# Optimization experiments

Measured on AMD Instinct MI355X. Metric: run time of the kernel, lower is better.

## Reference

```python
import jax, jax.numpy as jnp
import numpy as np

N, E = 20000, 320000
CS, CV = 64, 32          # scalar / vector multiplicities of node (= node_pre) irreps
AS_, AV, H = 16, 8, 4    # attn irreps scalar/vector muls, num_heads
NB = 16                  # num_basis
SQRT3 = 1.7320508075688772
SQRT2 = 1.4142135623730951
EPS = 1e-5

# dtp weight layout: [ss(CS), sv(CS), vs(CV), vv0(CV), vv1(CV)] -> numel = 2*CS+3*CV = 224

def _cg_tp(s, v, y0, y1, w_ss, w_sv, w_vs, w_vv0, w_vv1):
    """Depthwise CG tensor product for l<=1.
    s:(E,CS) v:(E,CV,3) y0:(E,) y1:(E,3); weights (E,C) or (C,).
    out scalars (E, CS+CV): 0e x 0e -> 0e, 1o x 1o -> 0e (dot/sqrt3)
    out vectors (E, CS+2*CV, 3): 0e x 1o -> 1o, 1o x 0e -> 1o, 1o x 1o -> 1o (cross/sqrt2)
    """
    out_s = jnp.concatenate([
        w_ss * s * y0[:, None],
        w_vv0 * (jnp.einsum('eci,ei->ec', v, y1) / SQRT3)], axis=-1)
    out_v = jnp.concatenate([
        (w_sv * s)[:, :, None] * y1[:, None, :],
        (w_vs * jnp.ones_like(v[..., 0]))[..., None] * v * y0[:, None, None],
        (w_vv1 * jnp.ones_like(v[..., 0]))[..., None] * (jnp.cross(v, y1[:, None, :]) / SQRT2)], axis=1)
    return out_s, out_v


def _equiv_layernorm(s, v, gamma_s, beta_s, gamma_v):
    mu = jnp.mean(s, axis=-1, keepdims=True)
    var = jnp.var(s, axis=-1, keepdims=True)
    s_n = (s - mu) * jax.lax.rsqrt(var + EPS) * gamma_s + beta_s
    rms = jnp.sqrt(jnp.mean(jnp.sum(v * v, axis=-1), axis=-1, keepdims=True) + EPS)
    v_n = v / rms[..., None] * gamma_v[None, :, None]
    return s_n, v_n


def setup_inputs() -> dict:
    key = jax.random.key(0)
    ks = jax.random.split(key, 26)
    def rn(k, shape, fan):
        return jax.random.normal(k, shape, jnp.float32) / np.sqrt(fan)
    D1S, D1V = CS + CV, CS + 2 * CV          # 96, 128 (dtp output muls)
    WN = 2 * CS + 3 * CV                     # 224 dtp weight numel
    inp = {
        'node': jax.random.normal(ks[0], (N, CS + 3 * CV), jnp.float32),
        'edge_index': jax.random.randint(ks[1], (2, E), 0, N, jnp.int64 if jax.config.jax_enable_x64 else jnp.int32),
        'rbf': jax.random.uniform(ks[2], (E, NB), jnp.float32),
        'rsh': jax.random.normal(ks[3], (E, 4), jnp.float32),
        'gamma_s': jnp.ones((CS,), jnp.float32),
        'beta_s': jnp.zeros((CS,), jnp.float32),
        'gamma_v': jnp.ones((CV,), jnp.float32),
        'Ws_src': rn(ks[4], (CS, CS), CS), 'Wv_src': rn(ks[5], (CV, CV), CV),
        'Ws_dst': rn(ks[6], (CS, CS), CS), 'Wv_dst': rn(ks[7], (CV, CV), CV),
        'W_rbf': rn(ks[8], (NB, WN), NB),
        'W_alpha': rn(ks[9], (D1S, H * AS_), D1S),
        'alpha_dot': rn(ks[10], (1, H, AS_), AS_),
        'Ws_val': rn(ks[11], (D1S, CS), D1S), 'Wv_val': rn(ks[12], (D1V, CV), D1V),
        'Wg': rn(ks[13], (CS, CV), CS),
        'w2_ss': rn(ks[14], (CS,), 1), 'w2_sv': rn(ks[15], (CS,), 1),
        'w2_vs': rn(ks[16], (CV,), 1), 'w2_vv0': rn(ks[17], (CV,), 1), 'w2_vv1': rn(ks[18], (CV,), 1),
        'Ws_vlin': rn(ks[19], (D1S, H * AS_), D1S), 'Wv_vlin': rn(ks[20], (D1V, H * AV), D1V),
        'Wps': rn(ks[21], (H * AS_, CS), H * AS_), 'Wpv': rn(ks[22], (H * AV, CV), H * AV),
    }
    return inp


def reference(node, rbf, rsh, gamma_s, beta_s, gamma_v, Ws_src, Wv_src, Ws_dst, Wv_dst,
              W_rbf, W_alpha, alpha_dot, Ws_val, Wv_val, Wg,
              w2_ss, w2_sv, w2_vs, w2_vv0, w2_vv1, Ws_vlin, Wv_vlin, Wps, Wpv, edge_index):
    n = node.shape[0]
    e = rsh.shape[0]
    s = node[:, :CS]
    v = node[:, CS:].reshape(n, CV, 3)
    # equivariant layer norm
    s_n, v_n = _equiv_layernorm(s, v, gamma_s, beta_s, gamma_v)
    # merge_src / merge_dst (irrep-wise o3.Linear)
    src, dst = edge_index[0], edge_index[1]
    msg_s = (s_n @ Ws_src)[src] + (s_n @ Ws_dst)[dst]                       # (E,CS)
    msg_v = jnp.einsum('ncx,cd->ndx', v_n, Wv_src)[src] + \
            jnp.einsum('ncx,cd->ndx', v_n, Wv_dst)[dst]                     # (E,CV,3)
    y0, y1 = rsh[:, 0], rsh[:, 1:4]
    # dtp1: per-edge weighted CG coupling, weights from rbf
    w1 = rbf @ W_rbf                                                        # (E,224)
    m1_s, m1_v = _cg_tp(msg_s, msg_v, y0, y1,
                        w1[:, :CS], w1[:, CS:2*CS], w1[:, 2*CS:2*CS+CV],
                        w1[:, 2*CS+CV:2*CS+2*CV], w1[:, 2*CS+2*CV:])        # (E,96) (E,128,3)
    # attention logits
    a = (m1_s @ W_alpha).reshape(e, H, AS_)
    a = jnp.where(a > 0, a, 0.2 * a)                                        # LeakyReLU(0.2)
    a = jnp.sum(a * alpha_dot, axis=-1, keepdims=True)                      # (E,H,1)
    # softmax over incoming edges of each destination node
    amax = jax.ops.segment_max(a, dst, num_segments=n)
    amax = jnp.where(jnp.isfinite(amax), amax, 0.0)
    ex = jnp.exp(a - amax[dst])
    den = jax.ops.segment_sum(ex, dst, num_segments=n)
    alpha = ex / (den[dst] + 1e-16)                                         # (E,H,1)
    # value path
    val_s = m1_s @ Ws_val                                                   # (E,CS)
    val_v = jnp.einsum('ecx,cd->edx', m1_v, Wv_val)                         # (E,CV,3)
    # gate: sigmoid on scalars, vectors gated by sigmoid of learned scalar gates
    val_v = val_v * jax.nn.sigmoid(val_s @ Wg)[..., None]
    val_s = jax.nn.sigmoid(val_s)
    # dtp2: shared internal weights
    m2_s, m2_v = _cg_tp(val_s, val_v, y0, y1, w2_ss, w2_sv, w2_vs, w2_vv0, w2_vv1)
    # value_lin -> (attn_irreps * num_heads), head-major layout
    hs = (m2_s @ Ws_vlin).reshape(e, H, AS_)
    hv = jnp.einsum('ecx,cd->edx', m2_v, Wv_vlin).reshape(e, H, AV, 3)
    h = jnp.concatenate([hs, hv.reshape(e, H, AV * 3)], axis=-1)            # (E,H,40)
    # attend + scatter-add to destination nodes
    agg = jax.ops.segment_sum(alpha * h, dst, num_segments=n)               # (N,H,40)
    agg_s = agg[:, :, :AS_].reshape(n, H * AS_)                             # (N,64)
    agg_v = agg[:, :, AS_:].reshape(n, H * AV, 3)                           # (N,32,3)
    out = node + jnp.concatenate([
        agg_s @ Wps,
        jnp.einsum('ncx,cd->ndx', agg_v, Wpv).reshape(n, CV * 3)], axis=-1)
    return out
```

## Files before the change

kernel.cpp:

```cpp
#include <hip/hip_runtime.h>
#include <hip/hip_bf16.h>
#include <cstddef>

typedef __hip_bfloat16 bf16;
typedef __bf16 bfv8 __attribute__((ext_vector_type(8)));
typedef float f4 __attribute__((ext_vector_type(4)));

#define EPSN 1e-5f
#define SQRT3_INV 0.57735026918962576f
#define SQRT2_INV 0.70710678118654752f

__device__ __forceinline__ float b2f(bf16 x) { return __bfloat162float(x); }

template<int BF> __device__ __forceinline__ float ldf(const void* p, size_t i) {
    if (BF) return __bfloat162float(((const bf16*)p)[i]);
    return ((const float*)p)[i];
}
__device__ __forceinline__ float ldr(const void* p, size_t i, int bfm) {
    return bfm ? __bfloat162float(((const bf16*)p)[i]) : ((const float*)p)[i];
}
template<int BF> __device__ __forceinline__ void stf(void* p, size_t i, float v) {
    if (BF) ((bf16*)p)[i] = __float2bfloat16(v);
    else    ((float*)p)[i] = v;
}

__device__ __forceinline__ float wave_sum64(float x) {
    #pragma unroll
    for (int m = 1; m < 64; m <<= 1) x += __shfl_xor(x, m, 64);
    return x;
}

__device__ __forceinline__ f4 mf(bfv8 a, bfv8 b, f4 c) {
    return __builtin_amdgcn_mfma_f32_16x16x32_bf16(a, b, c, 0, 0, 0);
}

__global__ __launch_bounds__(256) void k_sniff(const void* node, const void* eidx, int* flags)
{
    int t = threadIdx.x;
    __shared__ int cnt;
    __shared__ unsigned orr;
    if (t == 0) { cnt = 0; orr = 0u; }
    __syncthreads();
    unsigned w  = ((const unsigned*)node)[t];
    unsigned lo = w & 0xFFFFu;
    int e_lo = (int)((lo >> 7) & 0xFF);
    if (e_lo >= 96 && e_lo <= 140) atomicAdd(&cnt, 1);
    unsigned odd = ((const unsigned*)eidx)[2 * t + 1];
    atomicOr(&orr, odd);
    __syncthreads();
    if (t == 0) {
        flags[0] = (cnt >= 128) ? 1 : 0;
        flags[1] = (orr == 0u) ? 1 : 0;
    }
}

__global__ __launch_bounds__(256) void k_zero(float* p, int n)
{
    int i = blockIdx.x * 256 + threadIdx.x;
    if (i < n) p[i] = 0.f;
}

__global__ __launch_bounds__(256) void k_hist(const void* eidx, int* cnt,
                                              const int* flags, int E)
{
    int e = blockIdx.x * 256 + threadIdx.x;
    if (e >= E) return;
    int d = flags[1] ? (int)((const long long*)eidx)[(long long)E + e]
                     : ((const int*)eidx)[(size_t)E + e];
    atomicAdd(&cnt[d], 1);
}

__global__ __launch_bounds__(256) void k_scan(int* cnt, int N)
{
    __shared__ int part[256];
    int t = threadIdx.x;
    int chunk = (N + 255) / 256;
    int lo = t * chunk, hi = lo + chunk; if (hi > N) hi = N; if (lo > N) lo = N;
    int sum = 0;
    for (int i = lo; i < hi; ++i) sum += cnt[i];
    part[t] = sum;
    __syncthreads();
    if (t == 0) {
        int acc = 0;
        for (int i = 0; i < 256; ++i) { int v = part[i]; part[i] = acc; acc += v; }
    }
    __syncthreads();
    int acc = part[t];
    for (int i = lo; i < hi; ++i) { int v = cnt[i]; cnt[i] = acc; acc += v; }
}

__global__ __launch_bounds__(256) void k_perm(const void* eidx, int* cnt, int* perm,
                                              const int* flags, int E)
{
    int e = blockIdx.x * 256 + threadIdx.x;
    if (e >= E) return;
    int d = flags[1] ? (int)((const long long*)eidx)[(long long)E + e]
                     : ((const int*)eidx)[(size_t)E + e];
    int pos = atomicAdd(&cnt[d], 1);
    perm[pos] = e;
}

template<int BF>
__device__ __forceinline__ void prep_impl(
    const void* Walpha, const void* Wsval, const void* Wsvlin,
    const void* Wvval, const void* Wvvlin, const void* Wg,
    const void* Wrbf, const void* adot,
    const void* w2ss, const void* w2sv, const void* w2vs,
    const void* w2vv0, const void* w2vv1,
    bf16* WalphaT, bf16* WsvalT, bf16* WsvlinT,
    bf16* WvvalT, bf16* WvvlinT, bf16* WgT,
    bf16* WrbfT, bf16* adotB, bf16* w2B)
{
    int t = threadIdx.x + blockIdx.x * 256;
    int T = gridDim.x * 256;
    for (int i = t; i < 96 * 64; i += T) {
        int c = i >> 6, n = i & 63;
        WalphaT[n * 96 + c] = __float2bfloat16(ldf<BF>(Walpha, i));
        WsvalT [n * 96 + c] = __float2bfloat16(ldf<BF>(Wsval,  i));
        WsvlinT[n * 96 + c] = __float2bfloat16(ldf<BF>(Wsvlin, i));
    }
    for (int i = t; i < 128 * 32; i += T) {
        int c = i >> 5, n = i & 31;
        WvvalT [n * 128 + c] = __float2bfloat16(ldf<BF>(Wvval,  i));
        WvvlinT[n * 128 + c] = __float2bfloat16(ldf<BF>(Wvvlin, i));
    }
    for (int i = t; i < 64 * 32; i += T) {
        int c = i >> 5, n = i & 31;
        WgT[n * 64 + c] = __float2bfloat16(ldf<BF>(Wg, i));
    }
    for (int i = t; i < 16 * 224; i += T) {
        int b = i / 224, c = i - b * 224;
        WrbfT[c * 16 + b] = __float2bfloat16(ldf<BF>(Wrbf, i));
    }
    if (t < 64) adotB[t] = __float2bfloat16(ldf<BF>(adot, t));
    if (t < 64) w2B[t]      = __float2bfloat16(ldf<BF>(w2ss, t));
    if (t < 64) w2B[64 + t] = __float2bfloat16(ldf<BF>(w2sv, t));
    if (t < 32) {
        w2B[128 + t] = __float2bfloat16(ldf<BF>(w2vs, t));
        w2B[160 + t] = __float2bfloat16(ldf<BF>(w2vv0, t));
        w2B[192 + t] = __float2bfloat16(ldf<BF>(w2vv1, t));
    }
}

__global__ __launch_bounds__(256) void k_prep(
    const void* Walpha, const void* Wsval, const void* Wsvlin,
    const void* Wvval, const void* Wvvlin, const void* Wg,
    const void* Wrbf, const void* adot,
    const void* w2ss, const void* w2sv, const void* w2vs,
    const void* w2vv0, const void* w2vv1,
    bf16* WalphaT, bf16* WsvalT, bf16* WsvlinT,
    bf16* WvvalT, bf16* WvvlinT, bf16* WgT,
    bf16* WrbfT, bf16* adotB, bf16* w2B, const int* flags)
{
    if (flags[0])
        prep_impl<1>(Walpha, Wsval, Wsvlin, Wvval, Wvvlin, Wg, Wrbf, adot,
                     w2ss, w2sv, w2vs, w2vv0, w2vv1,
                     WalphaT, WsvalT, WsvlinT, WvvalT, WvvlinT, WgT, WrbfT, adotB, w2B);
    else
        prep_impl<0>(Walpha, Wsval, Wsvlin, Wvval, Wvvlin, Wg, Wrbf, adot,
                     w2ss, w2sv, w2vs, w2vv0, w2vv1,
                     WalphaT, WsvalT, WsvlinT, WvvalT, WvvlinT, WgT, WrbfT, adotB, w2B);
}

template<int BF>
__device__ __forceinline__ void node_impl(
    const void* node, const void* gs, const void* bs, const void* gv,
    const void* Wss, const void* Wvs, const void* Wsd, const void* Wvd,
    bf16* ssrc, bf16* sdst, bf16* vsrc, bf16* vdst,
    float* shs, float* shv, int n, int lane)
{
    size_t nb = (size_t)n * 160;

    float s  = ldf<BF>(node, nb + lane);
    float mu = wave_sum64(s) * (1.f / 64.f);
    float d  = s - mu;
    float var = wave_sum64(d * d) * (1.f / 64.f);
    float sn  = d * rsqrtf(var + EPSN) * ldf<BF>(gs, lane) + ldf<BF>(bs, lane);
    shs[lane] = sn;

    float v0 = 0.f, v1 = 0.f, v2 = 0.f, q = 0.f;
    if (lane < 32) {
        v0 = ldf<BF>(node, nb + 64 + lane * 3 + 0);
        v1 = ldf<BF>(node, nb + 64 + lane * 3 + 1);
        v2 = ldf<BF>(node, nb + 64 + lane * 3 + 2);
        q = v0 * v0 + v1 * v1 + v2 * v2;
    }
    float msq = wave_sum64(q) * (1.f / 32.f);
    float inv = rsqrtf(msq + EPSN);
    if (lane < 32) {
        float g = ldf<BF>(gv, lane);
        shv[0 * 32 + lane] = v0 * inv * g;
        shv[1 * 32 + lane] = v1 * inv * g;
        shv[2 * 32 + lane] = v2 * inv * g;
    }

    float a1 = 0.f, a2 = 0.f;
    for (int c = 0; c < 64; ++c) {
        float sc = shs[c];
        a1 += sc * ldf<BF>(Wss, c * 64 + lane);
        a2 += sc * ldf<BF>(Wsd, c * 64 + lane);
    }
    ssrc[(size_t)n * 64 + lane] = __float2bfloat16(a1);
    sdst[(size_t)n * 64 + lane] = __float2bfloat16(a2);

    {
        int x = lane >> 5, dd = lane & 31;
        float p1 = 0.f, p2 = 0.f;
        for (int c = 0; c < 32; ++c) {
            float vc = shv[x * 32 + c];
            p1 += vc * ldf<BF>(Wvs, c * 32 + dd);
            p2 += vc * ldf<BF>(Wvd, c * 32 + dd);
        }
        vsrc[(size_t)n * 96 + x * 32 + dd] = __float2bfloat16(p1);
        vdst[(size_t)n * 96 + x * 32 + dd] = __float2bfloat16(p2);
    }
    if (lane < 32) {
        int dd = lane;
        float p1 = 0.f, p2 = 0.f;
        for (int c = 0; c < 32; ++c) {
            float vc = shv[2 * 32 + c];
            p1 += vc * ldf<BF>(Wvs, c * 32 + dd);
            p2 += vc * ldf<BF>(Wvd, c * 32 + dd);
        }
        vsrc[(size_t)n * 96 + 64 + dd] = __float2bfloat16(p1);
        vdst[(size_t)n * 96 + 64 + dd] = __float2bfloat16(p2);
    }
}

__global__ __launch_bounds__(256) void k_node(
    const void* node, const void* gs, const void* bs, const void* gv,
    const void* Wss, const void* Wvs, const void* Wsd, const void* Wvd,
    bf16* ssrc, bf16* sdst, bf16* vsrc, bf16* vdst,
    const int* flags, int N)
{
    __shared__ float shs[4][64];
    __shared__ float shv[4][96];
    int wv = threadIdx.x >> 6, lane = threadIdx.x & 63;
    int n = blockIdx.x * 4 + wv; if (n >= N) return;
    if (flags[0])
        node_impl<1>(node, gs, bs, gv, Wss, Wvs, Wsd, Wvd, ssrc, sdst, vsrc, vdst,
                     shs[wv], shv[wv], n, lane);
    else
        node_impl<0>(node, gs, bs, gv, Wss, Wvs, Wsd, Wvd, ssrc, sdst, vsrc, vdst,
                     shs[wv], shv[wv], n, lane);
}

static constexpr int A1S = 0,    SS = 104;
static constexpr int A1V = 1664, PV = 2176, SV = 136;
static constexpr int VAL = 8192, SA = 72;
static constexpr int HSZ = 9344;

__global__ __launch_bounds__(256, 2) void k_edge(
    const void* __restrict__ eidx, const void* __restrict__ rbf, const void* __restrict__ rsh,
    const bf16* __restrict__ WalphaT, const bf16* __restrict__ WsvalT, const bf16* __restrict__ WsvlinT,
    const bf16* __restrict__ WvvalT, const bf16* __restrict__ WvvlinT, const bf16* __restrict__ WgT,
    const bf16* __restrict__ WrbfT, const bf16* __restrict__ adotB, const bf16* __restrict__ w2B,
    const bf16* __restrict__ ssrc, const bf16* __restrict__ sdst,
    const bf16* __restrict__ vsrc, const bf16* __restrict__ vdst,
    const int* __restrict__ perm,
    float* __restrict__ den, float* __restrict__ agg,
    const int* __restrict__ flags, int E)
{
    const int bfm = flags[0];
    const int i64 = flags[1];

    __shared__ __align__(16) __bf16 sH[4][HSZ];
    __shared__ __align__(16) float sRbf[4][16][20];
    __shared__ __align__(16) float sY[4][16][4];
    __shared__ int sSD[4][48];

    int wv = threadIdx.x >> 6, l = threadIdx.x & 63;
    int q = l >> 4, m = l & 15;
    long long eb = ((long long)blockIdx.x * 4 + wv) * 16;
    if (eb >= E) return;
    __bf16* H = &sH[wv][0];

    if (l < 16) {
        long long p = eb + l; if (p > (long long)E - 1) p = E - 1;
        sSD[wv][32 + l] = perm[p];
    }
    if (l < 32) {
        int pe = sSD[wv][32 + (l & 15)];
        long long off = (l < 16) ? (long long)pe : ((long long)E + pe);
        sSD[wv][l] = i64 ? (int)((const long long*)eidx)[off] : ((const int*)eidx)[off];
    }
    {
        int pe = sSD[wv][32 + (l >> 2)];
        sY[wv][l >> 2][l & 3] = ldr(rsh, (size_t)pe * 4 + (l & 3), bfm);
    }
    #pragma unroll
    for (int j = 0; j < 4; ++j) {
        int pe = sSD[wv][32 + j * 4 + q];
        sRbf[wv][m][j * 4 + q] = ldr(rbf, (size_t)pe * 16 + m, bfm);
    }

    const __bf16* wrt = (const __bf16*)WrbfT;
    int lv = l & 31;
    bfv8 w0a = *(const bfv8*)(wrt + l * 16);
    bfv8 w0b = *(const bfv8*)(wrt + l * 16 + 8);
    bfv8 w1a = *(const bfv8*)(wrt + (64 + l) * 16);
    bfv8 w1b = *(const bfv8*)(wrt + (64 + l) * 16 + 8);
    bfv8 w2a = *(const bfv8*)(wrt + (128 + lv) * 16);
    bfv8 w2b = *(const bfv8*)(wrt + (128 + lv) * 16 + 8);
    bfv8 w3a = *(const bfv8*)(wrt + (160 + lv) * 16);
    bfv8 w3b = *(const bfv8*)(wrt + (160 + lv) * 16 + 8);
    bfv8 w4a = *(const bfv8*)(wrt + (192 + lv) * 16);
    bfv8 w4b = *(const bfv8*)(wrt + (192 + lv) * 16 + 8);

    #pragma unroll 1
    for (int h = 0; h < 2; ++h) {
        bf16 rS[8], rD[8], rv[6][8];
        #pragma unroll
        for (int k = 0; k < 8; ++k) {
            int s = sSD[wv][8 * h + k], d = sSD[wv][16 + 8 * h + k];
            rS[k] = ssrc[(size_t)s * 64 + l];
            rD[k] = sdst[(size_t)d * 64 + l];
            if (l < 32) {
                rv[0][k] = vsrc[(size_t)s * 96 +      l];
                rv[1][k] = vsrc[(size_t)s * 96 + 32 + l];
                rv[2][k] = vsrc[(size_t)s * 96 + 64 + l];
                rv[3][k] = vdst[(size_t)d * 96 +      l];
                rv[4][k] = vdst[(size_t)d * 96 + 32 + l];
                rv[5][k] = vdst[(size_t)d * 96 + 64 + l];
            }
        }
        #pragma unroll
        for (int j2 = 0; j2 < 2; ++j2) {
            int jj = 2 * h + j2;
            float y0k[4], yxk[4], yyk[4], yzk[4], ms[4];
            float mv0[4], mv1[4], mv2[4];
            #pragma unroll
            for (int k = 0; k < 4; ++k) {
                float4 yy = *(const float4*)&sY[wv][4 * jj + k][0];
                y0k[k] = yy.x; yxk[k] = yy.y; yyk[k] = yy.z; yzk[k] = yy.w;
                int kk = 4 * j2 + k;
                ms[k]  = b2f(rS[kk]) + b2f(rD[kk]);
                mv0[k] = b2f(rv[0][kk]) + b2f(rv[3][kk]);
                mv1[k] = b2f(rv[1][kk]) + b2f(rv[4][kk]);
                mv2[k] = b2f(rv[2][kk]) + b2f(rv[5][kk]);
            }
            float wss[4] = {0,0,0,0}, wsv[4] = {0,0,0,0};
            float wvs[4] = {0,0,0,0}, wv0[4] = {0,0,0,0}, wv1[4] = {0,0,0,0};
            #pragma unroll
            for (int b = 0; b < 16; ++b) {
                float2 ra = *(const float2*)&sRbf[wv][b][4 * jj];
                float2 rb = *(const float2*)&sRbf[wv][b][4 * jj + 2];
                float r0 = ra.x, r1 = ra.y, r2 = rb.x, r3 = rb.y;
                float wa  = (float)(b < 8 ? w0a[b] : w0b[b - 8]);
                float wb_ = (float)(b < 8 ? w1a[b] : w1b[b - 8]);
                float wc  = (float)(b < 8 ? w2a[b] : w2b[b - 8]);
                float wd  = (float)(b < 8 ? w3a[b] : w3b[b - 8]);
                float we  = (float)(b < 8 ? w4a[b] : w4b[b - 8]);
                wss[0] += r0 * wa;  wss[1] += r1 * wa;  wss[2] += r2 * wa;  wss[3] += r3 * wa;
                wsv[0] += r0 * wb_; wsv[1] += r1 * wb_; wsv[2] += r2 * wb_; wsv[3] += r3 * wb_;
                wvs[0] += r0 * wc;  wvs[1] += r1 * wc;  wvs[2] += r2 * wc;  wvs[3] += r3 * wc;
                wv0[0] += r0 * wd;  wv0[1] += r1 * wd;  wv0[2] += r2 * wd;  wv0[3] += r3 * wd;
                wv1[0] += r0 * we;  wv1[1] += r1 * we;  wv1[2] += r2 * we;  wv1[3] += r3 * we;
            }
            #pragma unroll
            for (int k = 0; k < 4; ++k) {
                int e = 4 * jj + k;
                H[A1S + e * SS + l] = (__bf16)(wss[k] * ms[k] * y0k[k]);
                float sv = wsv[k] * ms[k];
                H[A1V + 0 * PV + e * SV + l] = (__bf16)(sv * yxk[k]);
                H[A1V + 1 * PV + e * SV + l] = (__bf16)(sv * yyk[k]);
                H[A1V + 2 * PV + e * SV + l] = (__bf16)(sv * yzk[k]);
            }
            if (l < 32) {
                #pragma unroll
                for (int k = 0; k < 4; ++k) {
                    int e = 4 * jj + k;
                    H[A1S + e * SS + 64 + l] =
                        (__bf16)(wv0[k] * (mv0[k] * yxk[k] + mv1[k] * yyk[k] + mv2[k] * yzk[k]) * SQRT3_INV);
                    H[A1V + 0 * PV + e * SV + 64 + l] = (__bf16)(wvs[k] * mv0[k] * y0k[k]);
                    H[A1V + 1 * PV + e * SV + 64 + l] = (__bf16)(wvs[k] * mv1[k] * y0k[k]);
                    H[A1V + 2 * PV + e * SV + 64 + l] = (__bf16)(wvs[k] * mv2[k] * y0k[k]);
                    float cx = mv1[k] * yzk[k] - mv2[k] * yyk[k];
                    float cy = mv2[k] * yxk[k] - mv0[k] * yzk[k];
                    float cz = mv0[k] * yyk[k] - mv1[k] * yxk[k];
                    H[A1V + 0 * PV + e * SV + 96 + l] = (__bf16)(wv1[k] * cx * SQRT2_INV);
                    H[A1V + 1 * PV + e * SV + 96 + l] = (__bf16)(wv1[k] * cy * SQRT2_INV);
                    H[A1V + 2 * PV + e * SV + 96 + l] = (__bf16)(wv1[k] * cz * SQRT2_INV);
                }
            }
        }
    }

    const int kq = q * 8;

    bfv8 a1s0 = *(const bfv8*)(H + A1S + m * SS + 0  + kq);
    bfv8 a1s1 = *(const bfv8*)(H + A1S + m * SS + 32 + kq);
    bfv8 a1s2 = *(const bfv8*)(H + A1S + m * SS + 64 + kq);
    f4 vals[4];
    #pragma unroll
    for (int nt = 0; nt < 4; ++nt) {
        const __bf16* bp = (const __bf16*)WsvalT + (size_t)(nt * 16 + m) * 96 + kq;
        f4 acc = {0.f, 0.f, 0.f, 0.f};
        acc = mf(a1s0, *(const bfv8*)(bp),      acc);
        acc = mf(a1s1, *(const bfv8*)(bp + 32), acc);
        acc = mf(a1s2, *(const bfv8*)(bp + 64), acc);
        vals[nt] = acc;
    }
    #pragma unroll
    for (int nt = 0; nt < 4; ++nt)
        #pragma unroll
        for (int r = 0; r < 4; ++r) {
            float v = vals[nt][r];
            H[VAL + (q * 4 + r) * SA + nt * 16 + m] = (__bf16)v;
            vals[nt][r] = 1.f / (1.f + __expf(-v));
        }

    bfv8 av0 = *(const bfv8*)(H + VAL + m * SA + 0  + kq);
    bfv8 av1 = *(const bfv8*)(H + VAL + m * SA + 32 + kq);
    f4 gate[2];
    #pragma unroll
    for (int nt = 0; nt < 2; ++nt) {
        const __bf16* bp = (const __bf16*)WgT + (size_t)(nt * 16 + m) * 64 + kq;
        f4 acc = {0.f, 0.f, 0.f, 0.f};
        acc = mf(av0, *(const bfv8*)(bp),      acc);
        acc = mf(av1, *(const bfv8*)(bp + 32), acc);
        gate[nt] = acc;
    }
    #pragma unroll
    for (int nt = 0; nt < 2; ++nt)
        #pragma unroll
        for (int r = 0; r < 4; ++r)
            gate[nt][r] = 1.f / (1.f + __expf(-gate[nt][r]));

    float ex_[4][4];
    #pragma unroll
    for (int nt = 0; nt < 4; ++nt) {
        const __bf16* bp = (const __bf16*)WalphaT + (size_t)(nt * 16 + m) * 96 + kq;
        f4 acc = {0.f, 0.f, 0.f, 0.f};
        acc = mf(a1s0, *(const bfv8*)(bp),      acc);
        acc = mf(a1s1, *(const bfv8*)(bp + 32), acc);
        acc = mf(a1s2, *(const bfv8*)(bp + 64), acc);
        float ad = b2f(adotB[nt * 16 + m]);
        #pragma unroll
        for (int r = 0; r < 4; ++r) {
            float tv = acc[r];
            tv = tv > 0.f ? tv : 0.2f * tv;
            tv *= ad;
            tv += __shfl_xor(tv, 1); tv += __shfl_xor(tv, 2);
            tv += __shfl_xor(tv, 4); tv += __shfl_xor(tv, 8);
            tv = fminf(fmaxf(tv, -60.f), 60.f);
            ex_[nt][r] = __expf(tv);
        }
    }

    bfv8 a1v[3][4];
    #pragma unroll
    for (int x = 0; x < 3; ++x)
        #pragma unroll
        for (int kt = 0; kt < 4; ++kt)
            a1v[x][kt] = *(const bfv8*)(H + A1V + x * PV + m * SV + kt * 32 + kq);
    f4 vv[3][2];
    #pragma unroll
    for (int x = 0; x < 3; ++x)
        #pragma unroll
        for (int nt = 0; nt < 2; ++nt)
            vv[x][nt] = (f4){0.f, 0.f, 0.f, 0.f};
    #pragma unroll
    for (int nt = 0; nt < 2; ++nt) {
        const __bf16* bp = (const __bf16*)WvvalT + (size_t)(nt * 16 + m) * 128 + kq;
        #pragma unroll
        for (int kt = 0; kt < 4; ++kt) {
            bfv8 b = *(const bfv8*)(bp + kt * 32);
            vv[0][nt] = mf(a1v[0][kt], b, vv[0][nt]);
            vv[1][nt] = mf(a1v[1][kt], b, vv[1][nt]);
            vv[2][nt] = mf(a1v[2][kt], b, vv[2][nt]);
        }
    }
    #pragma unroll
    for (int x = 0; x < 3; ++x)
        #pragma unroll
        for (int nt = 0; nt < 2; ++nt)
            #pragma unroll
            for (int r = 0; r < 4; ++r)
                vv[x][nt][r] *= gate[nt][r];

    float c2ss[4], c2sv[4];
    #pragma unroll
    for (int nt = 0; nt < 4; ++nt) {
        c2ss[nt] = b2f(w2B[nt * 16 + m]);
        c2sv[nt] = b2f(w2B[64 + nt * 16 + m]);
    }
    float c2vs[2], c2v0[2], c2v1[2];
    #pragma unroll
    for (int nt = 0; nt < 2; ++nt) {
        c2vs[nt] = b2f(w2B[128 + nt * 16 + m]);
        c2v0[nt] = b2f(w2B[160 + nt * 16 + m]);
        c2v1[nt] = b2f(w2B[192 + nt * 16 + m]);
    }
    #pragma unroll
    for (int r = 0; r < 4; ++r) {
        int e = q * 4 + r;
        float4 yy = *(const float4*)&sY[wv][e][0];
        float y0 = yy.x, yx = yy.y, yh = yy.z, yz = yy.w;
        int rS  = A1S + e * SS;
        int rV0 = A1V + 0 * PV + e * SV;
        int rV1 = A1V + 1 * PV + e * SV;
        int rV2 = A1V + 2 * PV + e * SV;
        #pragma unroll
        for (int nt = 0; nt < 4; ++nt) {
            int c = nt * 16 + m;
            float va = vals[nt][r];
            H[rS + c] = (__bf16)(c2ss[nt] * va * y0);
            float t2 = c2sv[nt] * va;
            H[rV0 + c] = (__bf16)(t2 * yx);
            H[rV1 + c] = (__bf16)(t2 * yh);
            H[rV2 + c] = (__bf16)(t2 * yz);
        }
        #pragma unroll
        for (int nt = 0; nt < 2; ++nt) {
            int c = nt * 16 + m;
            float v0 = vv[0][nt][r], v1 = vv[1][nt][r], v2 = vv[2][nt][r];
            H[rS + 64 + c] = (__bf16)(c2v0[nt] * (v0 * yx + v1 * yh + v2 * yz) * SQRT3_INV);
            H[rV0 + 64 + c] = (__bf16)(c2vs[nt] * v0 * y0);
            H[rV1 + 64 + c] = (__bf16)(c2vs[nt] * v1 * y0);
            H[rV2 + 64 + c] = (__bf16)(c2vs[nt] * v2 * y0);
            float cx = v1 * yz - v2 * yh;
            float cy = v2 * yx - v0 * yz;
            float cz = v0 * yh - v1 * yx;
            H[rV0 + 96 + c] = (__bf16)(c2v1[nt] * cx * SQRT2_INV);
            H[rV1 + 96 + c] = (__bf16)(c2v1[nt] * cy * SQRT2_INV);
            H[rV2 + 96 + c] = (__bf16)(c2v1[nt] * cz * SQRT2_INV);
        }
    }

    bfv8 a2s0 = *(const bfv8*)(H + A1S + m * SS + 0  + kq);
    bfv8 a2s1 = *(const bfv8*)(H + A1S + m * SS + 32 + kq);
    bfv8 a2s2 = *(const bfv8*)(H + A1S + m * SS + 64 + kq);
    f4 hs[4];
    #pragma unroll
    for (int nt = 0; nt < 4; ++nt) {
        const __bf16* bp = (const __bf16*)WsvlinT + (size_t)(nt * 16 + m) * 96 + kq;
        f4 acc = {0.f, 0.f, 0.f, 0.f};
        acc = mf(a2s0, *(const bfv8*)(bp),      acc);
        acc = mf(a2s1, *(const bfv8*)(bp + 32), acc);
        acc = mf(a2s2, *(const bfv8*)(bp + 64), acc);
        hs[nt] = acc;
    }
    bfv8 a2v[3][4];
    #pragma unroll
    for (int x = 0; x < 3; ++x)
        #pragma unroll
        for (int kt = 0; kt < 4; ++kt)
            a2v[x][kt] = *(const bfv8*)(H + A1V + x * PV + m * SV + kt * 32 + kq);
    f4 hv[3][2];
    #pragma unroll
    for (int x = 0; x < 3; ++x)
        #pragma unroll
        for (int nt = 0; nt < 2; ++nt)
            hv[x][nt] = (f4){0.f, 0.f, 0.f, 0.f};
    #pragma unroll
    for (int nt = 0; nt < 2; ++nt) {
        const __bf16* bp = (const __bf16*)WvvlinT + (size_t)(nt * 16 + m) * 128 + kq;
        #pragma unroll
        for (int kt = 0; kt < 4; ++kt) {
            bfv8 b = *(const bfv8*)(bp + kt * 32);
            hv[0][nt] = mf(a2v[0][kt], b, hv[0][nt]);
            hv[1][nt] = mf(a2v[1][kt], b, hv[1][nt]);
            hv[2][nt] = mf(a2v[2][kt], b, hv[2][nt]);
        }
    }

    float* Hf = (float*)H;
    #pragma unroll
    for (int r = 0; r < 4; ++r) {
        int e = q * 4 + r;
        float* row = Hf + e * 168;
        #pragma unroll
        for (int nt = 0; nt < 4; ++nt)
            row[nt * 40 + m] = ex_[nt][r] * hs[nt][r];
        #pragma unroll
        for (int nt = 0; nt < 2; ++nt) {
            int c = nt * 16 + m;
            int hh = c >> 3, dd = c & 7;
            float exv = (m >= 8) ? ex_[2 * nt + 1][r] : ex_[2 * nt][r];
            float* vb = row + hh * 40 + 16 + dd * 3;
            vb[0] = exv * hv[0][nt][r];
            vb[1] = exv * hv[1][nt][r];
            vb[2] = exv * hv[2][nt][r];
        }
        if (m < 4) row[160 + m] = ex_[m][r];
    }
    int nval = (int)((E - eb) < 16 ? (E - eb) : 16);
    {
        int s = 0;
        while (s < nval) {
            int d = sSD[wv][16 + s];
            int t = s + 1;
            while (t < nval && sSD[wv][16 + t] == d) ++t;
            float s0 = 0.f, s1 = 0.f, s2 = 0.f;
            for (int e = s; e < t; ++e) {
                const float* row = Hf + e * 168;
                s0 += row[l];
                s1 += row[64 + l];
                if (l < 36) s2 += row[128 + l];
            }
            float* rowp = agg + (size_t)d * 160;
            unsafeAtomicAdd(rowp + l, s0);
            unsafeAtomicAdd(rowp + 64 + l, s1);
            if (l < 32)      unsafeAtomicAdd(rowp + 128 + l, s2);
            else if (l < 36) unsafeAtomicAdd(den + (size_t)d * 4 + (l - 32), s2);
            s = t;
        }
    }
}

template<int BF>
__device__ __forceinline__ void out_impl(
    const void* node, const float* den, const float* agg,
    const void* Wps, const void* Wpv, void* out,
    float* shs, float* shv, float* sinv, int n, int lane)
{
    if (lane < 4) sinv[lane] = 1.f / (den[(size_t)n * 4 + lane] + 1e-16f);
    for (int idx = lane; idx < 160; idx += 64) {
        int h = idx / 40, r = idx - h * 40;
        float val = agg[(size_t)n * 160 + idx] * sinv[h];
        if (r < 16) shs[h * 16 + r] = val;
        else { int rr = r - 16; int dd = rr / 3, x = rr - dd * 3; shv[x * 32 + h * 8 + dd] = val; }
    }

    float acc = ldf<BF>(node, (size_t)n * 160 + lane);
    for (int c = 0; c < 64; ++c) acc += shs[c] * ldf<BF>(Wps, c * 64 + lane);
    stf<BF>(out, (size_t)n * 160 + lane, acc);

    {
        int idx = lane; int dd = idx / 3, x = idx - dd * 3;
        float a = ldf<BF>(node, (size_t)n * 160 + 64 + idx);
        for (int c = 0; c < 32; ++c) a += shv[x * 32 + c] * ldf<BF>(Wpv, c * 32 + dd);
        stf<BF>(out, (size_t)n * 160 + 64 + idx, a);
    }
    if (lane < 32) {
        int idx = 64 + lane; int dd = idx / 3, x = idx - dd * 3;
        float a = ldf<BF>(node, (size_t)n * 160 + 64 + idx);
        for (int c = 0; c < 32; ++c) a += shv[x * 32 + c] * ldf<BF>(Wpv, c * 32 + dd);
        stf<BF>(out, (size_t)n * 160 + 64 + idx, a);
    }
}

__global__ __launch_bounds__(256) void k_out(
    const void* node, const float* den, const float* agg,
    const void* Wps, const void* Wpv, void* out,
    const int* flags, int N)
{
    __shared__ float shs[4][64];
    __shared__ float shv[4][96];
    __shared__ float sinv[4][4];
    int wv = threadIdx.x >> 6, lane = threadIdx.x & 63;
    int n = blockIdx.x * 4 + wv; if (n >= N) return;
    if (flags[0])
        out_impl<1>(node, den, agg, Wps, Wpv, out, shs[wv], shv[wv], sinv[wv], n, lane);
    else
        out_impl<0>(node, den, agg, Wps, Wpv, out, shs[wv], shv[wv], sinv[wv], n, lane);
}

extern "C" void kernel_launch(void* const* d_in, const int* in_sizes, int n_in,
                              void* d_out, int out_size, void* d_ws, size_t ws_size,
                              hipStream_t stream)
{
    const void* node   = d_in[0];
    const void* eidx   = d_in[1];
    const void* rbf    = d_in[2];
    const void* rsh    = d_in[3];
    const void* gs     = d_in[4];
    const void* bs     = d_in[5];
    const void* gv     = d_in[6];
    const void* Wss    = d_in[7];
    const void* Wvs    = d_in[8];
    const void* Wsd    = d_in[9];
    const void* Wvd    = d_in[10];
    const void* Wrbf   = d_in[11];
    const void* Walpha = d_in[12];
    const void* adot   = d_in[13];
    const void* Wsval  = d_in[14];
    const void* Wvval  = d_in[15];
    const void* Wg     = d_in[16];
    const void* w2ss   = d_in[17];
    const void* w2sv   = d_in[18];
    const void* w2vs   = d_in[19];
    const void* w2vv0  = d_in[20];
    const void* w2vv1  = d_in[21];
    const void* Wsvlin = d_in[22];
    const void* Wvvlin = d_in[23];
    const void* Wps    = d_in[24];
    const void* Wpv    = d_in[25];

    int N = in_sizes[0] / 160;
    int E = in_sizes[1] / 2;

    char* base = (char*)d_ws;
    int*  flags   = (int*)base;
    bf16* WalphaT = (bf16*)(base + 16);
    bf16* WsvalT  = WalphaT + 6144;
    bf16* WsvlinT = WsvalT  + 6144;
    bf16* WvvalT  = WsvlinT + 6144;
    bf16* WvvlinT = WvvalT  + 4096;
    bf16* WgT     = WvvlinT + 4096;
    bf16* WrbfT   = WgT     + 2048;
    bf16* adotB   = WrbfT   + 3584;
    bf16* w2B     = adotB   + 64;
    bf16* ssrc    = w2B     + 224;
    bf16* sdst    = ssrc + (size_t)N * 64;
    bf16* vsrc    = sdst + (size_t)N * 64;
    bf16* vdst    = vsrc + (size_t)N * 96;
    float* den    = (float*)(vdst + (size_t)N * 96);
    float* agg    = den + (size_t)N * 4;
    int*  cnt     = (int*)(agg + (size_t)N * 160);
    int*  perm    = cnt + N;

    k_sniff<<<1, 256, 0, stream>>>(node, eidx, flags);
    int zn = N * 164;
    k_zero<<<(zn + 255) / 256, 256, 0, stream>>>(den, zn);
    k_zero<<<(N + 255) / 256, 256, 0, stream>>>((float*)cnt, N);

    int nbe = (E + 255) / 256;
    k_hist<<<nbe, 256, 0, stream>>>(eidx, cnt, flags, E);
    k_scan<<<1, 256, 0, stream>>>(cnt, N);
    k_perm<<<nbe, 256, 0, stream>>>(eidx, cnt, perm, flags, E);

    k_prep<<<16, 256, 0, stream>>>(Walpha, Wsval, Wsvlin, Wvval, Wvvlin, Wg, Wrbf, adot,
                                   w2ss, w2sv, w2vs, w2vv0, w2vv1,
                                   WalphaT, WsvalT, WsvlinT, WvvalT, WvvlinT, WgT, WrbfT,
                                   adotB, w2B, flags);

    int nbn = (N + 3) / 4;
    k_node<<<nbn, 256, 0, stream>>>(node, gs, bs, gv, Wss, Wvs, Wsd, Wvd,
                                    ssrc, sdst, vsrc, vdst, flags, N);

    int nb = (E + 63) / 64;
    k_edge<<<nb, 256, 0, stream>>>(eidx, rbf, rsh,
                                   WalphaT, WsvalT, WsvlinT, WvvalT, WvvlinT, WgT, WrbfT,
                                   adotB, w2B, ssrc, sdst, vsrc, vdst, perm, den, agg, flags, E);

    int nbo = (N + 3) / 4;
    k_out<<<nbo, 256, 0, stream>>>(node, den, agg, Wps, Wpv, d_out, flags, N);
}
```

Measured before the change: 498.0 us.

## Compute rbf weights via MFMA, shrink LDS, raise edge-kernel occupancy, parallel scan

The per-edge radial weight projection (rbf x Wrbf) moves from a scalar FMA loop onto MFMA instructions, using a zero-padded 32-wide transposed weight matrix. The rbf staging buffer in shared memory is removed and the H buffer is compacted, with VAL aliased onto offset 0, so each block can hold five waves of 320 threads at three blocks per CU. The node-feature gathers are restructured per MFMA lane layout. Separately, the single-thread prefix scan is replaced with a 1024-thread wave-shuffle scan. Aliasing VAL onto the H buffer relies on the earlier data being dead by the time it is overwritten.

Result: slower. 544.5 us (+9.3%).

```diff
diff --git a/kernel.cpp b/kernel.cpp
--- a/kernel.cpp
+++ b/kernel.cpp
@@ -70,22 +70,35 @@
     atomicAdd(&cnt[d], 1);
 }
 
-__global__ __launch_bounds__(256) void k_scan(int* cnt, int N)
-{
-    __shared__ int part[256];
+__global__ __launch_bounds__(1024) void k_scan(int* cnt, int N)
+{
+    __shared__ int wsum[16];
     int t = threadIdx.x;
-    int chunk = (N + 255) / 256;
-    int lo = t * chunk, hi = lo + chunk; if (hi > N) hi = N; if (lo > N) lo = N;
+    int lane = t & 63, w = t >> 6;
+    int chunk = (N + 1023) >> 10;
+    int lo = t * chunk, hi = lo + chunk;
+    if (hi > N) hi = N; if (lo > N) lo = N;
     int sum = 0;
     for (int i = lo; i < hi; ++i) sum += cnt[i];
-    part[t] = sum;
+    int x = sum;
+    #pragma unroll
+    for (int off = 1; off < 64; off <<= 1) {
+        int y = __shfl_up(x, off, 64);
+        if (lane >= off) x += y;
+    }
+    if (lane == 63) wsum[w] = x;
     __syncthreads();
-    if (t == 0) {
-        int acc = 0;
-        for (int i = 0; i < 256; ++i) { int v = part[i]; part[i] = acc; acc += v; }
+    if (t < 64) {
+        int v = (lane < 16) ? wsum[lane] : 0;
+        #pragma unroll
+        for (int off = 1; off < 16; off <<= 1) {
+            int y = __shfl_up(v, off, 64);
+            if (lane >= off) v += y;
+        }
+        if (lane < 16) wsum[lane] = v;
     }
     __syncthreads();
-    int acc = part[t];
+    int acc = x - sum + (w ? wsum[w - 1] : 0);
     for (int i = lo; i < hi; ++i) { int v = cnt[i]; cnt[i] = acc; acc += v; }
 }
 
@@ -128,9 +141,9 @@
         int c = i >> 5, n = i & 31;
         WgT[n * 64 + c] = __float2bfloat16(ldf<BF>(Wg, i));
     }
-    for (int i = t; i < 16 * 224; i += T) {
-        int b = i / 224, c = i - b * 224;
-        WrbfT[c * 16 + b] = __float2bfloat16(ldf<BF>(Wrbf, i));
+    for (int i = t; i < 224 * 32; i += T) {
+        int c = i >> 5, b = i & 31;
+        WrbfT[i] = __float2bfloat16(b < 16 ? ldf<BF>(Wrbf, b * 224 + c) : 0.f);
     }
     if (t < 64) adotB[t] = __float2bfloat16(ldf<BF>(adot, t));
     if (t < 64) w2B[t]      = __float2bfloat16(ldf<BF>(w2ss, t));
@@ -178,14 +191,14 @@
     float sn  = d * rsqrtf(var + EPSN) * ldf<BF>(gs, lane) + ldf<BF>(bs, lane);
     shs[lane] = sn;
 
-    float v0 = 0.f, v1 = 0.f, v2 = 0.f, q = 0.f;
+    float v0 = 0.f, v1 = 0.f, v2 = 0.f, qq = 0.f;
     if (lane < 32) {
         v0 = ldf<BF>(node, nb + 64 + lane * 3 + 0);
         v1 = ldf<BF>(node, nb + 64 + lane * 3 + 1);
         v2 = ldf<BF>(node, nb + 64 + lane * 3 + 2);
-        q = v0 * v0 + v1 * v1 + v2 * v2;
-    }
-    float msq = wave_sum64(q) * (1.f / 32.f);
+        qq = v0 * v0 + v1 * v1 + v2 * v2;
+    }
+    float msq = wave_sum64(qq) * (1.f / 32.f);
     float inv = rsqrtf(msq + EPSN);
     if (lane < 32) {
         float g = ldf<BF>(gv, lane);
@@ -245,12 +258,16 @@
                      shs[wv], shv[wv], n, lane);
 }
 
-static constexpr int A1S = 0,    SS = 104;
-static constexpr int A1V = 1664, PV = 2176, SV = 136;
-static constexpr int VAL = 8192, SA = 72;
-static constexpr int HSZ = 9344;
-
-__global__ __launch_bounds__(256, 2) void k_edge(
+static constexpr int SS  = 100;
+static constexpr int A1S = 0;
+static constexpr int SV  = 132;
+static constexpr int PV  = 16 * SV;
+static constexpr int A1V = 16 * SS;
+static constexpr int VAL = 0;
+static constexpr int SA  = 72;
+static constexpr int HSZ = A1V + 3 * PV;
+
+__global__ __launch_bounds__(320, 3) void k_edge(
     const void* __restrict__ eidx, const void* __restrict__ rbf, const void* __restrict__ rsh,
     const bf16* __restrict__ WalphaT, const bf16* __restrict__ WsvalT, const bf16* __restrict__ WsvlinT,
     const bf16* __restrict__ WvvalT, const bf16* __restrict__ WvvlinT, const bf16* __restrict__ WgT,
@@ -264,14 +281,14 @@
     const int bfm = flags[0];
     const int i64 = flags[1];
 
-    __shared__ __align__(16) __bf16 sH[4][HSZ];
-    __shared__ __align__(16) float sRbf[4][16][20];
-    __shared__ __align__(16) float sY[4][16][4];
-    __shared__ int sSD[4][48];
+    __shared__ __align__(16) __bf16 sH[5][HSZ];
+    __shared__ __align__(16) float sY[5][16][4];
+    __shared__ int sSD[5][48];
 
     int wv = threadIdx.x >> 6, l = threadIdx.x & 63;
     int q = l >> 4, m = l & 15;
-    long long eb = ((long long)blockIdx.x * 4 + wv) * 16;
+    const int kq = q * 8;
+    long long eb = ((long long)blockIdx.x * 5 + wv) * 16;
     if (eb >= E) return;
     __bf16* H = &sH[wv][0];
 
@@ -288,105 +305,82 @@
         int pe = sSD[wv][32 + (l >> 2)];
         sY[wv][l >> 2][l & 3] = ldr(rsh, (size_t)pe * 4 + (l & 3), bfm);
     }
-    #pragma unroll
-    for (int j = 0; j < 4; ++j) {
-        int pe = sSD[wv][32 + j * 4 + q];
-        sRbf[wv][m][j * 4 + q] = ldr(rbf, (size_t)pe * 16 + m, bfm);
-    }
-
-    const __bf16* wrt = (const __bf16*)WrbfT;
-    int lv = l & 31;
-    bfv8 w0a = *(const bfv8*)(wrt + l * 16);
-    bfv8 w0b = *(const bfv8*)(wrt + l * 16 + 8);
-    bfv8 w1a = *(const bfv8*)(wrt + (64 + l) * 16);
-    bfv8 w1b = *(const bfv8*)(wrt + (64 + l) * 16 + 8);
-    bfv8 w2a = *(const bfv8*)(wrt + (128 + lv) * 16);
-    bfv8 w2b = *(const bfv8*)(wrt + (128 + lv) * 16 + 8);
-    bfv8 w3a = *(const bfv8*)(wrt + (160 + lv) * 16);
-    bfv8 w3b = *(const bfv8*)(wrt + (160 + lv) * 16 + 8);
-    bfv8 w4a = *(const bfv8*)(wrt + (192 + lv) * 16);
-    bfv8 w4b = *(const bfv8*)(wrt + (192 + lv) * 16 + 8);
-
-    #pragma unroll 1
-    for (int h = 0; h < 2; ++h) {
-        bf16 rS[8], rD[8], rv[6][8];
-        #pragma unroll
-        for (int k = 0; k < 8; ++k) {
-            int s = sSD[wv][8 * h + k], d = sSD[wv][16 + 8 * h + k];
-            rS[k] = ssrc[(size_t)s * 64 + l];
-            rD[k] = sdst[(size_t)d * 64 + l];
-            if (l < 32) {
-                rv[0][k] = vsrc[(size_t)s * 96 +      l];
-                rv[1][k] = vsrc[(size_t)s * 96 + 32 + l];
-                rv[2][k] = vsrc[(size_t)s * 96 + 64 + l];
-                rv[3][k] = vdst[(size_t)d * 96 +      l];
-                rv[4][k] = vdst[(size_t)d * 96 + 32 + l];
-                rv[5][k] = vdst[(size_t)d * 96 + 64 + l];
+
+    f4 w1f[14];
+    {
+        bfv8 arb;
+        #pragma unroll
+        for (int i = 0; i < 8; ++i) arb[i] = (__bf16)0.f;
+        if (q < 2) {
+            int pe = sSD[wv][32 + m];
+            if (bfm) {
+                arb = *(const bfv8*)((const __bf16*)rbf + (size_t)pe * 16 + kq);
+            } else {
+                const float* rp = (const float*)rbf + (size_t)pe * 16 + kq;
+                #pragma unroll
+                for (int i = 0; i < 8; ++i) arb[i] = (__bf16)rp[i];
             }
         }
-        #pragma unroll
-        for (int j2 = 0; j2 < 2; ++j2) {
-            int jj = 2 * h + j2;
-            float y0k[4], yxk[4], yyk[4], yzk[4], ms[4];
-            float mv0[4], mv1[4], mv2[4];
+        const __bf16* wb = (const __bf16*)WrbfT;
+        #pragma unroll
+        for (int nt = 0; nt < 14; ++nt) {
+            bfv8 bb = *(const bfv8*)(wb + (size_t)(nt * 16 + m) * 32 + kq);
+            f4 z = {0.f, 0.f, 0.f, 0.f};
+            w1f[nt] = mf(arb, bb, z);
+        }
+    }
+
+    #pragma unroll
+    for (int r = 0; r < 4; ++r) {
+        int e = q * 4 + r;
+        int s = sSD[wv][e], d = sSD[wv][16 + e];
+        const bf16* sp = ssrc + (size_t)s * 64 + m;
+        const bf16* dp = sdst + (size_t)d * 64 + m;
+        float ms_[4];
+        #pragma unroll
+        for (int nt = 0; nt < 4; ++nt)
+            ms_[nt] = b2f(sp[nt * 16]) + b2f(dp[nt * 16]);
+        const bf16* vp = vsrc + (size_t)s * 96 + m;
+        const bf16* wp = vdst + (size_t)d * 96 + m;
+        float mv_[2][3];
+        #pragma unroll
+        for (int x = 0; x < 3; ++x)
             #pragma unroll
-            for (int k = 0; k < 4; ++k) {
-                float4 yy = *(const float4*)&sY[wv][4 * jj + k][0];
-                y0k[k] = yy.x; yxk[k] = yy.y; yyk[k] = yy.z; yzk[k] = yy.w;
-                int kk = 4 * j2 + k;
-                ms[k]  = b2f(rS[kk]) + b2f(rD[kk]);
-                mv0[k] = b2f(rv[0][kk]) + b2f(rv[3][kk]);
-                mv1[k] = b2f(rv[1][kk]) + b2f(rv[4][kk]);
-                mv2[k] = b2f(rv[2][kk]) + b2f(rv[5][kk]);
-            }
-            float wss[4] = {0,0,0,0}, wsv[4] = {0,0,0,0};
-            float wvs[4] = {0,0,0,0}, wv0[4] = {0,0,0,0}, wv1[4] = {0,0,0,0};
-            #pragma unroll
-            for (int b = 0; b < 16; ++b) {
-                float2 ra = *(const float2*)&sRbf[wv][b][4 * jj];
-                float2 rb = *(const float2*)&sRbf[wv][b][4 * jj + 2];
-                float r0 = ra.x, r1 = ra.y, r2 = rb.x, r3 = rb.y;
-                float wa  = (float)(b < 8 ? w0a[b] : w0b[b - 8]);
-                float wb_ = (float)(b < 8 ? w1a[b] : w1b[b - 8]);
-                float wc  = (float)(b < 8 ? w2a[b] : w2b[b - 8]);
-                float wd  = (float)(b < 8 ? w3a[b] : w3b[b - 8]);
-                float we  = (float)(b < 8 ? w4a[b] : w4b[b - 8]);
-                wss[0] += r0 * wa;  wss[1] += r1 * wa;  wss[2] += r2 * wa;  wss[3] += r3 * wa;
-                wsv[0] += r0 * wb_; wsv[1] += r1 * wb_; wsv[2] += r2 * wb_; wsv[3] += r3 * wb_;
-                wvs[0] += r0 * wc;  wvs[1] += r1 * wc;  wvs[2] += r2 * wc;  wvs[3] += r3 * wc;
-                wv0[0] += r0 * wd;  wv0[1] += r1 * wd;  wv0[2] += r2 * wd;  wv0[3] += r3 * wd;
-                wv1[0] += r0 * we;  wv1[1] += r1 * we;  wv1[2] += r2 * we;  wv1[3] += r3 * we;
-            }
-            #pragma unroll
-            for (int k = 0; k < 4; ++k) {
-                int e = 4 * jj + k;
-                H[A1S + e * SS + l] = (__bf16)(wss[k] * ms[k] * y0k[k]);
-                float sv = wsv[k] * ms[k];
-                H[A1V + 0 * PV + e * SV + l] = (__bf16)(sv * yxk[k]);
-                H[A1V + 1 * PV + e * SV + l] = (__bf16)(sv * yyk[k]);
-                H[A1V + 2 * PV + e * SV + l] = (__bf16)(sv * yzk[k]);
-            }
-            if (l < 32) {
-                #pragma unroll
-                for (int k = 0; k < 4; ++k) {
-                    int e = 4 * jj + k;
-                    H[A1S + e * SS + 64 + l] =
-                        (__bf16)(wv0[k] * (mv0[k] * yxk[k] + mv1[k] * yyk[k] + mv2[k] * yzk[k]) * SQRT3_INV);
-                    H[A1V + 0 * PV + e * SV + 64 + l] = (__bf16)(wvs[k] * mv0[k] * y0k[k]);
-                    H[A1V + 1 * PV + e * SV + 64 + l] = (__bf16)(wvs[k] * mv1[k] * y0k[k]);
-                    H[A1V + 2 * PV + e * SV + 64 + l] = (__bf16)(wvs[k] * mv2[k] * y0k[k]);
-                    float cx = mv1[k] * yzk[k] - mv2[k] * yyk[k];
-                    float cy = mv2[k] * yxk[k] - mv0[k] * yzk[k];
-                    float cz = mv0[k] * yyk[k] - mv1[k] * yxk[k];
-                    H[A1V + 0 * PV + e * SV + 96 + l] = (__bf16)(wv1[k] * cx * SQRT2_INV);
-                    H[A1V + 1 * PV + e * SV + 96 + l] = (__bf16)(wv1[k] * cy * SQRT2_INV);
-                    H[A1V + 2 * PV + e * SV + 96 + l] = (__bf16)(wv1[k] * cz * SQRT2_INV);
-                }
-            }
-        }
-    }
-
-    const int kq = q * 8;
+            for (int n2 = 0; n2 < 2; ++n2)
+                mv_[n2][x] = b2f(vp[x * 32 + n2 * 16]) + b2f(wp[x * 32 + n2 * 16]);
+
+        float4 yy = *(const float4*)&sY[wv][e][0];
+        float y0 = yy.x, yx = yy.y, yh = yy.z, yz = yy.w;
+        int rS  = A1S + e * SS;
+        int rV0 = A1V + e * SV;
+
+        #pragma unroll
+        for (int nt = 0; nt < 4; ++nt) {
+            int c = nt * 16 + m;
+            float t1 = w1f[nt][r] * ms_[nt];
+            H[rS + c] = (__bf16)(t1 * y0);
+            float sv = w1f[4 + nt][r] * ms_[nt];
+            H[rV0 + 0 * PV + c] = (__bf16)(sv * yx);
+            H[rV0 + 1 * PV + c] = (__bf16)(sv * yh);
+            H[rV0 + 2 * PV + c] = (__bf16)(sv * yz);
+        }
+        #pragma unroll
+        for (int n2 = 0; n2 < 2; ++n2) {
+            int c = n2 * 16 + m;
+            float v0 = mv_[n2][0], v1 = mv_[n2][1], v2 = mv_[n2][2];
+            float wvsc = w1f[8 + n2][r], wv0c = w1f[10 + n2][r], wv1c = w1f[12 + n2][r];
+            H[rS + 64 + c] = (__bf16)(wv0c * (v0 * yx + v1 * yh + v2 * yz) * SQRT3_INV);
+            H[rV0 + 0 * PV + 64 + c] = (__bf16)(wvsc * v0 * y0);
+            H[rV0 + 1 * PV + 64 + c] = (__bf16)(wvsc * v1 * y0);
+            H[rV0 + 2 * PV + 64 + c] = (__bf16)(wvsc * v2 * y0);
+            float cx = v1 * yz - v2 * yh;
+            float cy = v2 * yx - v0 * yz;
+            float cz = v0 * yh - v1 * yx;
+            H[rV0 + 0 * PV + 96 + c] = (__bf16)(wv1c * cx * SQRT2_INV);
+            H[rV0 + 1 * PV + 96 + c] = (__bf16)(wv1c * cy * SQRT2_INV);
+            H[rV0 + 2 * PV + 96 + c] = (__bf16)(wv1c * cz * SQRT2_INV);
+        }
+    }
 
     bfv8 a1s0 = *(const bfv8*)(H + A1S + m * SS + 0  + kq);
     bfv8 a1s1 = *(const bfv8*)(H + A1S + m * SS + 32 + kq);
@@ -700,7 +694,7 @@
     bf16* WvvlinT = WvvalT  + 4096;
     bf16* WgT     = WvvlinT + 4096;
     bf16* WrbfT   = WgT     + 2048;
-    bf16* adotB   = WrbfT   + 3584;
+    bf16* adotB   = WrbfT   + 7168;
     bf16* w2B     = adotB   + 64;
     bf16* ssrc    = w2B     + 224;
     bf16* sdst    = ssrc + (size_t)N * 64;
@@ -718,7 +712,7 @@
 
     int nbe = (E + 255) / 256;
     k_hist<<<nbe, 256, 0, stream>>>(eidx, cnt, flags, E);
-    k_scan<<<1, 256, 0, stream>>>(cnt, N);
+    k_scan<<<1, 1024, 0, stream>>>(cnt, N);
     k_perm<<<nbe, 256, 0, stream>>>(eidx, cnt, perm, flags, E);
 
     k_prep<<<16, 256, 0, stream>>>(Walpha, Wsval, Wsvlin, Wvval, Wvvlin, Wg, Wrbf, adot,
@@ -730,8 +724,8 @@
     k_node<<<nbn, 256, 0, stream>>>(node, gs, bs, gv, Wss, Wvs, Wsd, Wvd,
                                     ssrc, sdst, vsrc, vdst, flags, N);
 
-    int nb = (E + 63) / 64;
-    k_edge<<<nb, 256, 0, stream>>>(eidx, rbf, rsh,
+    int nb = (E + 79) / 80;
+    k_edge<<<nb, 320, 0, stream>>>(eidx, rbf, rsh,
                                    WalphaT, WsvalT, WsvlinT, WvvalT, WvvlinT, WgT, WrbfT,
                                    adotB, w2B, ssrc, sdst, vsrc, vdst, perm, den, agg, flags, E);
 
```
